# Performance work log

Measured on AMD Instinct MI355X. Metric: run time of the kernel, lower is better.

Reference implementation:

```python
import jax, jax.numpy as jnp
import numpy as np

N = 50000
E = 800000


def setup_inputs() -> dict:
    key = jax.random.key(0)
    ks = jax.random.split(key, 12)
    d, pd, h, md, od = 64, 3, 128, 64, 64

    def glorot(k, shape):
        fan_in = shape[0]
        return jax.random.normal(k, shape, dtype=jnp.float32) / jnp.sqrt(jnp.float32(fan_in))

    return {
        "x": jax.random.normal(ks[0], (N, d), dtype=jnp.float32),
        "pos": jax.random.normal(ks[1], (N, pd), dtype=jnp.float32),
        "edge_index": jax.random.randint(ks[2], (2, E), 0, N, dtype=jnp.int64 if jax.config.jax_enable_x64 else jnp.int32),
        "W1": glorot(ks[3], (2 * d + pd, h)),
        "b1": jnp.zeros((h,), dtype=jnp.float32),
        "W2": glorot(ks[4], (h, md)),
        "b2": jnp.zeros((md,), dtype=jnp.float32),
        "W3": glorot(ks[5], (d + md, h)),
        "b3": jnp.zeros((h,), dtype=jnp.float32),
        "W4": glorot(ks[6], (h, od)),
        "b4": jnp.zeros((od,), dtype=jnp.float32),
    }


def reference(x, pos, edge_index, W1, b1, W2, b2, W3, b3, W4, b4):
    # flow='target_to_source': i = edge_index[0] (aggregation node), j = edge_index[1]
    idx_i = edge_index[0]
    idx_j = edge_index[1]

    x_i = x[idx_i]          # [E, d]
    x_j = x[idx_j]          # [E, d]
    rel_pos = pos[idx_j] - pos[idx_i]  # [E, pd]  (neighbor_loc='position')

    # message MLP
    msg_in = jnp.concatenate([x_i, x_j - x_i, rel_pos], axis=1)  # [E, 2d+pd]
    hmsg = jax.nn.relu(msg_in @ W1 + b1)
    msg = hmsg @ W2 + b2  # [E, md]

    # scatter-mean aggregation at node i
    num_nodes = x.shape[0]
    summed = jax.ops.segment_sum(msg, idx_i, num_segments=num_nodes)  # [N, md]
    counts = jax.ops.segment_sum(jnp.ones((msg.shape[0],), dtype=msg.dtype), idx_i, num_segments=num_nodes)
    aggr = summed / jnp.maximum(counts, 1.0)[:, None]

    # update MLP (self_val=True: concat own features)
    upd_in = jnp.concatenate([x, aggr], axis=1)  # [N, d+md]
    hupd = jax.nn.relu(upd_in @ W3 + b3)
    return hupd @ W4 + b4  # [N, od]
```

## Files before the change

kernel.cpp:

```cpp
#include <hip/hip_runtime.h>


#define EPB 128
#define NPB 64

typedef __attribute__((ext_vector_type(8))) short bf16x8;
typedef __attribute__((ext_vector_type(4))) float f32x4;

static __device__ __forceinline__ unsigned short f2bf(float f) {
    union { float f; unsigned u; } v; v.f = f;
    unsigned u = v.u + 0x7FFFu + ((v.u >> 16) & 1u);
    return (unsigned short)(u >> 16);
}
static __device__ __forceinline__ float bf2f(unsigned short h) {
    union { unsigned u; float f; } v; v.u = ((unsigned)h) << 16;
    return v.f;
}
static __device__ __forceinline__ unsigned relu_add_pk(unsigned pu, unsigned qu) {
    union { unsigned u; float f; } plo, phi, qlo, qhi, lo, hi;
    plo.u = pu << 16;           phi.u = pu & 0xffff0000u;
    qlo.u = qu << 16;           qhi.u = qu & 0xffff0000u;
    lo.f = fmaxf(plo.f + qlo.f, 0.f);
    hi.f = fmaxf(phi.f + qhi.f, 0.f);
    return (hi.u & 0xffff0000u) | (lo.u >> 16);
}


__global__ __launch_bounds__(256) void count_kernel(
    const int* __restrict__ ei0, int* __restrict__ cnt,
    int* __restrict__ rank, int E)
{
    int e = blockIdx.x * 256 + threadIdx.x;
    if (e < E) rank[e] = atomicAdd(&cnt[ei0[e]], 1);
}

__global__ __launch_bounds__(1024) void scanA_kernel(
    const int* __restrict__ cnt, int* __restrict__ bsum, int N)
{
    __shared__ int ws[16];
    const int i = blockIdx.x * 1024 + threadIdx.x;
    int v = (i < N) ? cnt[i] : 0;
    #pragma unroll
    for (int d = 32; d >= 1; d >>= 1) v += __shfl_down(v, d, 64);
    if ((threadIdx.x & 63) == 0) ws[threadIdx.x >> 6] = v;
    __syncthreads();
    if (threadIdx.x == 0) {
        int s = 0;
        #pragma unroll
        for (int k = 0; k < 16; ++k) s += ws[k];
        bsum[blockIdx.x] = s;
    }
}

__global__ __launch_bounds__(1024) void scanC_kernel(
    const int* __restrict__ cnt, const int* __restrict__ bsum,
    int* __restrict__ off, int N, int Etot)
{
    __shared__ int wsum[16];
    __shared__ int boffs;
    const int i = blockIdx.x * 1024 + threadIdx.x;
    const int lane = threadIdx.x & 63, w = threadIdx.x >> 6;
    if (threadIdx.x < 64) {
        int acc = 0;
        for (int k = threadIdx.x; k < blockIdx.x; k += 64) acc += bsum[k];
        #pragma unroll
        for (int d = 32; d >= 1; d >>= 1) acc += __shfl_down(acc, d, 64);
        if (threadIdx.x == 0) boffs = acc;
    }
    const int v = (i < N) ? cnt[i] : 0;
    int incl = v;
    #pragma unroll
    for (int d = 1; d < 64; d <<= 1) {
        int t = __shfl_up(incl, d, 64);
        if (lane >= d) incl += t;
    }
    if (lane == 63) wsum[w] = incl;
    __syncthreads();
    int pre = 0;
    for (int k = 0; k < w; ++k) pre += wsum[k];
    if (i < N) off[i] = boffs + pre + incl - v;
    if (blockIdx.x == 0 && threadIdx.x == 0) off[N] = Etot;
}

__global__ __launch_bounds__(256) void fill_kernel(
    const int* __restrict__ ei0, const int* __restrict__ ei1,
    const int* __restrict__ off, const int* __restrict__ rank,
    int2* __restrict__ eij, int E)
{
    int e = blockIdx.x * 256 + threadIdx.x;
    if (e < E) {
        const int i = ei0[e];
        int2 v; v.x = i; v.y = ei1[e];
        eij[off[i] + rank[e]] = v;
    }
}


__global__ __launch_bounds__(64) void pack_weights_kernel(
    const float* __restrict__ W1, const float* __restrict__ W2,
    const float* __restrict__ W3, const float* __restrict__ W4,
    unsigned short* __restrict__ Wcp, unsigned short* __restrict__ W2p,
    unsigned short* __restrict__ W3p, unsigned short* __restrict__ W4p)
{
    int f = blockIdx.x;
    const int lane = threadIdx.x;
    if (f < 48) {
        const int nt = f / 3, ks = f % 3;
        const int n  = nt * 16 + (lane & 15);
        const int k0 = ks * 32 + (lane >> 4) * 8;
        unsigned short* dst = Wcp + (size_t)f * 512 + lane * 8;
        #pragma unroll
        for (int j = 0; j < 8; ++j) {
            const int k = k0 + j;
            float v = 0.f;
            if (n < 128) {
                if (k < 64)       v = W1[(size_t)k * 128 + n] - W1[(size_t)(64 + k) * 128 + n];
                else if (k < 67)  v = -W1[(size_t)(128 + k - 64) * 128 + n];
            } else {
                const int nq = n - 128;
                if (k < 64)       v = W1[(size_t)(64 + k) * 128 + nq];
                else if (k < 67)  v = W1[(size_t)(128 + k - 64) * 128 + nq];
            }
            dst[j] = f2bf(v);
        }
        return;
    }
    const float* W; unsigned short* out; int K, N, KS;
    if (f < 64)      { W = W2; out = W2p; K = 128; N = 64;  KS = 4; f -= 48; }
    else if (f < 96) { W = W3; out = W3p; K = 128; N = 128; KS = 4; f -= 64; }
    else             { W = W4; out = W4p; K = 128; N = 64;  KS = 4; f -= 96; }
    const int nt = f / KS, ks = f % KS;
    const int n  = nt * 16 + (lane & 15);
    const int k0 = ks * 32 + (lane >> 4) * 8;
    unsigned short* dst = out + (size_t)f * 512 + lane * 8;
    #pragma unroll
    for (int j = 0; j < 8; ++j) {
        float v = (k0 + j < K) ? W[(size_t)(k0 + j) * N + n] : 0.f;
        dst[j] = f2bf(v);
    }
}


__global__ __launch_bounds__(256) void pq_kernel(
    const float* __restrict__ x, const float* __restrict__ pos,
    const unsigned short* __restrict__ Wcp, const float* __restrict__ b1,
    unsigned short* __restrict__ P, unsigned short* __restrict__ Q, int N)
{
    __shared__ unsigned short s[NPB][136];

    const int tid  = threadIdx.x;
    const int wv   = tid >> 6;
    const int lane = tid & 63;
    const int r    = lane >> 4;
    const int c    = lane & 15;
    const int base = blockIdx.x * NPB;

    for (int nl = wv; nl < NPB; nl += 4) {
        const int n = base + nl;
        s[nl][lane] = (n < N) ? f2bf(x[(size_t)n * 64 + lane]) : 0;
        if (lane < 32)
            s[nl][64 + lane] = (n < N && lane < 3) ? f2bf(pos[(size_t)n * 3 + lane]) : 0;
    }
    __syncthreads();

    bf16x8 a[3];
    #pragma unroll
    for (int ks = 0; ks < 3; ++ks)
        a[ks] = *(const bf16x8*)&s[wv * 16 + c][ks * 32 + r * 8];
    __syncthreads();

    f32x4 acc[16];
    #pragma unroll
    for (int nt = 0; nt < 16; ++nt) {
        const float bv = (nt < 8) ? b1[nt * 16 + c] : 0.f;
        acc[nt] = (f32x4){bv, bv, bv, bv};
    }
    #pragma unroll
    for (int nt = 0; nt < 16; ++nt)
        #pragma unroll
        for (int ks = 0; ks < 3; ++ks) {
            const bf16x8 b = *(const bf16x8*)(Wcp + (size_t)(nt * 3 + ks) * 512 + lane * 8);
            acc[nt] = __builtin_amdgcn_mfma_f32_16x16x32_bf16(a[ks], b, acc[nt], 0, 0, 0);
        }

    #pragma unroll
    for (int nt = 0; nt < 8; ++nt)
        #pragma unroll
        for (int reg = 0; reg < 4; ++reg)
            s[wv * 16 + r * 4 + reg][nt * 16 + c] = f2bf(acc[nt][reg]);
    __syncthreads();
    {
        const int nl = tid >> 2, q = tid & 3;
        const int n = base + nl;
        if (n < N) {
            const ushort4* src = (const ushort4*)&s[nl][0];
            ushort4* dst = (ushort4*)(P + (size_t)n * 128);
            #pragma unroll
            for (int u = 0; u < 8; ++u) dst[q * 8 + u] = src[q * 8 + u];
        }
    }
    __syncthreads();

    #pragma unroll
    for (int nt = 8; nt < 16; ++nt)
        #pragma unroll
        for (int reg = 0; reg < 4; ++reg)
            s[wv * 16 + r * 4 + reg][(nt - 8) * 16 + c] = f2bf(acc[nt][reg]);
    __syncthreads();
    {
        const int nl = tid >> 2, q = tid & 3;
        const int n = base + nl;
        if (n < N) {
            const ushort4* src = (const ushort4*)&s[nl][0];
            ushort4* dst = (ushort4*)(Q + (size_t)n * 128);
            #pragma unroll
            for (int u = 0; u < 8; ++u) dst[q * 8 + u] = src[q * 8 + u];
        }
    }
}


__global__ __launch_bounds__(256) void edge_aggr_mfma(
    const unsigned short* __restrict__ P, const unsigned short* __restrict__ Q,
    const int2* __restrict__ eij,
    const unsigned short* __restrict__ W2p, const float* __restrict__ b2,
    float* __restrict__ aggr, int E)
{
    __shared__ unsigned short s_m[EPB][72];
    __shared__ int2 s_ij[EPB];
    __shared__ int  s_start[EPB + 4];
    __shared__ int  s_wsumA[2];
    __shared__ int  s_nruns;

    const int tid  = threadIdx.x;
    const int wv   = tid >> 6;
    const int lane = tid & 63;
    const int r    = lane >> 4;
    const int c    = lane & 15;
    const int base = blockIdx.x * EPB;
    const int ne   = min(EPB, E - base);

    if (tid < EPB) {
        const int p = base + tid;
        int2 v; v.x = -1; v.y = -1;
        if (p < E) v = eij[p];
        s_ij[tid] = v;
    }
    __syncthreads();

    bf16x8 a2[2][4];
    #pragma unroll
    for (int mh = 0; mh < 2; ++mh) {
        const int2 ij = s_ij[wv * 32 + mh * 16 + c];
        if (ij.x >= 0) {
            const unsigned* Pi = (const unsigned*)(P + (size_t)ij.x * 128);
            const unsigned* Qj = (const unsigned*)(Q + (size_t)ij.y * 128);
            #pragma unroll
            for (int ks = 0; ks < 4; ++ks) {
                const uint4 pu = *(const uint4*)(Pi + ks * 16 + r * 4);
                const uint4 qu = *(const uint4*)(Qj + ks * 16 + r * 4);
                uint4 h;
                h.x = relu_add_pk(pu.x, qu.x);
                h.y = relu_add_pk(pu.y, qu.y);
                h.z = relu_add_pk(pu.z, qu.z);
                h.w = relu_add_pk(pu.w, qu.w);
                a2[mh][ks] = *(const bf16x8*)&h;
            }
        } else {
            #pragma unroll
            for (int ks = 0; ks < 4; ++ks) a2[mh][ks] = (bf16x8){0,0,0,0,0,0,0,0};
        }
    }

    f32x4 acc2[2][4];
    #pragma unroll
    for (int nt = 0; nt < 4; ++nt) {
        const float bv = b2[nt * 16 + c];
        acc2[0][nt] = (f32x4){bv, bv, bv, bv};
        acc2[1][nt] = (f32x4){bv, bv, bv, bv};
    }
    #pragma unroll
    for (int nt = 0; nt < 4; ++nt)
        #pragma unroll
        for (int ks = 0; ks < 4; ++ks) {
            const bf16x8 b = *(const bf16x8*)(W2p + (size_t)(nt * 4 + ks) * 512 + lane * 8);
            acc2[0][nt] = __builtin_amdgcn_mfma_f32_16x16x32_bf16(a2[0][ks], b, acc2[0][nt], 0, 0, 0);
            acc2[1][nt] = __builtin_amdgcn_mfma_f32_16x16x32_bf16(a2[1][ks], b, acc2[1][nt], 0, 0, 0);
        }

    #pragma unroll
    for (int mh = 0; mh < 2; ++mh)
        #pragma unroll
        for (int nt = 0; nt < 4; ++nt)
            #pragma unroll
            for (int reg = 0; reg < 4; ++reg) {
                const int row = wv * 32 + mh * 16 + r * 4 + reg;
                s_m[row][nt * 16 + c] = f2bf(acc2[mh][nt][reg]);
            }

    int flag = 0, incl = 0;
    if (tid < EPB) {
        flag = (tid < ne) && (tid == 0 || s_ij[tid].x != s_ij[tid - 1].x);
        incl = flag;
    }
    #pragma unroll
    for (int d = 1; d < 64; d <<= 1) {
        int t = __shfl_up(incl, d, 64);
        if (lane >= d) incl += t;
    }
    if (tid < EPB && lane == 63) s_wsumA[tid >> 6] = incl;
    __syncthreads();
    if (tid < EPB) {
        const int rid = incl + ((tid >= 64) ? s_wsumA[0] : 0);
        if (flag) s_start[rid - 1] = tid;
    }
    if (tid == 0) {
        const int nr = s_wsumA[0] + s_wsumA[1];
        s_nruns = nr;
        s_start[nr] = ne;
    }
    __syncthreads();

    for (int rn = wv; rn < s_nruns; rn += 4) {
        const int e0 = s_start[rn], e1 = s_start[rn + 1];
        const int i  = s_ij[e0].x;
        float acc = 0.f;
        for (int e = e0; e < e1; ++e)
            acc += bf2f(s_m[e][lane]);
        atomicAdd(&aggr[(size_t)i * 64 + lane], acc);
    }
}


__global__ __launch_bounds__(256) void node_mlp_mfma(
    const float* __restrict__ x, const float* __restrict__ aggr,
    const int* __restrict__ off,
    const unsigned short* __restrict__ W3p, const float* __restrict__ b3,
    const unsigned short* __restrict__ W4p, const float* __restrict__ b4,
    float* __restrict__ out, int N)
{
    __shared__ unsigned short s_a[NPB][136];

    const int tid  = threadIdx.x;
    const int wv   = tid >> 6;
    const int lane = tid & 63;
    const int r    = lane >> 4;
    const int c    = lane & 15;
    const int base = blockIdx.x * NPB;

    for (int nl = wv; nl < NPB; nl += 4) {
        const int n = base + nl;
        if (n < N) {
            s_a[nl][lane] = f2bf(x[(size_t)n * 64 + lane]);
            const int deg = off[n + 1] - off[n];
            const float a = aggr[(size_t)n * 64 + lane] / (float)max(deg, 1);
            s_a[nl][64 + lane] = f2bf(a);
        } else {
            s_a[nl][lane] = 0;
            s_a[nl][64 + lane] = 0;
        }
    }
    __syncthreads();

    bf16x8 a1[4];
    #pragma unroll
    for (int ks = 0; ks < 4; ++ks)
        a1[ks] = *(const bf16x8*)&s_a[wv * 16 + c][ks * 32 + r * 8];
    __syncthreads();

    f32x4 acc1[8];
    #pragma unroll
    for (int nt = 0; nt < 8; ++nt) {
        const float bv = b3[nt * 16 + c];
        acc1[nt] = (f32x4){bv, bv, bv, bv};
    }
    #pragma unroll
    for (int nt = 0; nt < 8; ++nt)
        #pragma unroll
        for (int ks = 0; ks < 4; ++ks) {
            const bf16x8 b = *(const bf16x8*)(W3p + (size_t)(nt * 4 + ks) * 512 + lane * 8);
            acc1[nt] = __builtin_amdgcn_mfma_f32_16x16x32_bf16(a1[ks], b, acc1[nt], 0, 0, 0);
        }
    #pragma unroll
    for (int nt = 0; nt < 8; ++nt)
        #pragma unroll
        for (int reg = 0; reg < 4; ++reg)
            s_a[wv * 16 + r * 4 + reg][nt * 16 + c] = f2bf(fmaxf(acc1[nt][reg], 0.f));
    __syncthreads();

    bf16x8 a2[4];
    #pragma unroll
    for (int ks = 0; ks < 4; ++ks)
        a2[ks] = *(const bf16x8*)&s_a[wv * 16 + c][ks * 32 + r * 8];
    __syncthreads();

    f32x4 acc2[4];
    #pragma unroll
    for (int nt = 0; nt < 4; ++nt) {
        const float bv = b4[nt * 16 + c];
        acc2[nt] = (f32x4){bv, bv, bv, bv};
    }
    #pragma unroll
    for (int nt = 0; nt < 4; ++nt)
        #pragma unroll
        for (int ks = 0; ks < 4; ++ks) {
            const bf16x8 b = *(const bf16x8*)(W4p + (size_t)(nt * 4 + ks) * 512 + lane * 8);
            acc2[nt] = __builtin_amdgcn_mfma_f32_16x16x32_bf16(a2[ks], b, acc2[nt], 0, 0, 0);
        }

    #pragma unroll
    for (int nt = 0; nt < 4; ++nt)
        #pragma unroll
        for (int reg = 0; reg < 4; ++reg) {
            float* row = (float*)&s_a[wv * 16 + r * 4 + reg][0];
            row[nt * 16 + c] = acc2[nt][reg];
        }
    __syncthreads();

    {
        const int nl = tid >> 2, q = tid & 3;
        const int n = base + nl;
        if (n < N) {
            const float4* src = (const float4*)((const float*)&s_a[nl][0] + q * 16);
            float4* dst = (float4*)(out + (size_t)n * 64 + q * 16);
            #pragma unroll
            for (int u = 0; u < 4; ++u) dst[u] = src[u];
        }
    }
}


#define EB 32
#define NB 32

__global__ __launch_bounds__(256) void mpnn_edge_atomic_kernel(
    const float* __restrict__ x, const float* __restrict__ pos,
    const int* __restrict__ ei0, const int* __restrict__ ei1,
    const float* __restrict__ W1, const float* __restrict__ b1,
    const float* __restrict__ W2, const float* __restrict__ b2,
    float* __restrict__ summed, float* __restrict__ counts, int E)
{
    __shared__ float s_in[EB][132];
    __shared__ int   s_idx[EB];

    const int tid  = threadIdx.x;
    const int base = blockIdx.x * EB;
    const int wv   = tid >> 6;
    const int lane = tid & 63;

    for (int e = wv; e < EB; e += 4) {
        const int ei = base + e;
        if (ei < E) {
            const int i = ei0[ei];
            const int j = ei1[ei];
            const float xi = x[(size_t)i * 64 + lane];
            const float xj = x[(size_t)j * 64 + lane];
            s_in[e][lane]      = xi;
            s_in[e][64 + lane] = xj - xi;
            if (lane < 3)
                s_in[e][128 + lane] = pos[(size_t)j * 3 + lane] - pos[(size_t)i * 3 + lane];
            if (lane == 0) s_idx[e] = i;
        } else {
            s_in[e][lane] = 0.f; s_in[e][64 + lane] = 0.f;
            if (lane < 3) s_in[e][128 + lane] = 0.f;
            if (lane == 0) s_idx[e] = -1;
        }
    }
    __syncthreads();

    float acc1[4][4];
    {
        const int cg = tid & 31;
        const int er = tid >> 5;
        const float4 bb = *(const float4*)(b1 + 4 * cg);
        #pragma unroll
        for (int t = 0; t < 4; ++t) {
            acc1[t][0] = bb.x; acc1[t][1] = bb.y; acc1[t][2] = bb.z; acc1[t][3] = bb.w;
        }
        for (int k = 0; k < 128; k += 4) {
            float wv4[4][4];
            #pragma unroll
            for (int kk = 0; kk < 4; ++kk) {
                const float4 w = *(const float4*)(W1 + (size_t)(k + kk) * 128 + 4 * cg);
                wv4[kk][0] = w.x; wv4[kk][1] = w.y; wv4[kk][2] = w.z; wv4[kk][3] = w.w;
            }
            #pragma unroll
            for (int t = 0; t < 4; ++t) {
                const float4 m = *(const float4*)(&s_in[er + 8 * t][k]);
                const float mm[4] = {m.x, m.y, m.z, m.w};
                #pragma unroll
                for (int kk = 0; kk < 4; ++kk)
                    #pragma unroll
                    for (int cc = 0; cc < 4; ++cc)
                        acc1[t][cc] += mm[kk] * wv4[kk][cc];
            }
        }
        for (int k = 128; k < 131; ++k) {
            float wk[4];
            #pragma unroll
            for (int cc = 0; cc < 4; ++cc) wk[cc] = W1[(size_t)k * 128 + 4 * cg + cc];
            #pragma unroll
            for (int t = 0; t < 4; ++t) {
                const float m = s_in[er + 8 * t][k];
                #pragma unroll
                for (int cc = 0; cc < 4; ++cc) acc1[t][cc] += m * wk[cc];
            }
        }
    }
    __syncthreads();
    {
        const int cg = tid & 31;
        const int er = tid >> 5;
        #pragma unroll
        for (int t = 0; t < 4; ++t)
            #pragma unroll
            for (int cc = 0; cc < 4; ++cc)
                s_in[er + 8 * t][4 * cg + cc] = fmaxf(acc1[t][cc], 0.f);
    }
    __syncthreads();
    {
        const int cg = tid & 15;
        const int er = tid >> 4;
        float acc[2][4];
        const float4 bb = *(const float4*)(b2 + 4 * cg);
        #pragma unroll
        for (int t = 0; t < 2; ++t) {
            acc[t][0] = bb.x; acc[t][1] = bb.y; acc[t][2] = bb.z; acc[t][3] = bb.w;
        }
        for (int k = 0; k < 128; k += 4) {
            float wv4[4][4];
            #pragma unroll
            for (int kk = 0; kk < 4; ++kk) {
                const float4 w = *(const float4*)(W2 + (size_t)(k + kk) * 64 + 4 * cg);
                wv4[kk][0] = w.x; wv4[kk][1] = w.y; wv4[kk][2] = w.z; wv4[kk][3] = w.w;
            }
            #pragma unroll
            for (int t = 0; t < 2; ++t) {
                const float4 m = *(const float4*)(&s_in[er + 16 * t][k]);
                const float mm[4] = {m.x, m.y, m.z, m.w};
                #pragma unroll
                for (int kk = 0; kk < 4; ++kk)
                    #pragma unroll
                    for (int cc = 0; cc < 4; ++cc)
                        acc[t][cc] += mm[kk] * wv4[kk][cc];
            }
        }
        #pragma unroll
        for (int t = 0; t < 2; ++t) {
            const int e = er + 16 * t;
            const int i = s_idx[e];
            if (i >= 0) {
                #pragma unroll
                for (int cc = 0; cc < 4; ++cc)
                    atomicAdd(&summed[(size_t)i * 64 + 4 * cg + cc], acc[t][cc]);
            }
        }
    }
    if (tid < EB) {
        const int i = s_idx[tid];
        if (i >= 0) atomicAdd(&counts[i], 1.0f);
    }
}

__global__ __launch_bounds__(256) void mpnn_node_legacy_kernel(
    const float* __restrict__ x, const float* __restrict__ summed,
    const float* __restrict__ counts,
    const float* __restrict__ W3, const float* __restrict__ b3,
    const float* __restrict__ W4, const float* __restrict__ b4,
    float* __restrict__ out, int N)
{
    __shared__ float s_in[NB][132];

    const int tid  = threadIdx.x;
    const int base = blockIdx.x * NB;
    const int wv   = tid >> 6;
    const int lane = tid & 63;

    for (int nl = wv; nl < NB; nl += 4) {
        const int n = base + nl;
        if (n < N) {
            s_in[nl][lane] = x[(size_t)n * 64 + lane];
            const float inv = 1.0f / fmaxf(counts[n], 1.0f);
            s_in[nl][64 + lane] = summed[(size_t)n * 64 + lane] * inv;
        } else {
            s_in[nl][lane] = 0.f; s_in[nl][64 + lane] = 0.f;
        }
    }
    __syncthreads();

    float acc1[4][4];
    {
        const int cg = tid & 31;
        const int er = tid >> 5;
        const float4 bb = *(const float4*)(b3 + 4 * cg);
        #pragma unroll
        for (int t = 0; t < 4; ++t) {
            acc1[t][0] = bb.x; acc1[t][1] = bb.y; acc1[t][2] = bb.z; acc1[t][3] = bb.w;
        }
        for (int k = 0; k < 128; k += 4) {
            float wv4[4][4];
            #pragma unroll
            for (int kk = 0; kk < 4; ++kk) {
                const float4 w = *(const float4*)(W3 + (size_t)(k + kk) * 128 + 4 * cg);
                wv4[kk][0] = w.x; wv4[kk][1] = w.y; wv4[kk][2] = w.z; wv4[kk][3] = w.w;
            }
            #pragma unroll
            for (int t = 0; t < 4; ++t) {
                const float4 m = *(const float4*)(&s_in[er + 8 * t][k]);
                const float mm[4] = {m.x, m.y, m.z, m.w};
                #pragma unroll
                for (int kk = 0; kk < 4; ++kk)
                    #pragma unroll
                    for (int cc = 0; cc < 4; ++cc)
                        acc1[t][cc] += mm[kk] * wv4[kk][cc];
            }
        }
    }
    __syncthreads();
    {
        const int cg = tid & 31;
        const int er = tid >> 5;
        #pragma unroll
        for (int t = 0; t < 4; ++t)
            #pragma unroll
            for (int cc = 0; cc < 4; ++cc)
                s_in[er + 8 * t][4 * cg + cc] = fmaxf(acc1[t][cc], 0.f);
    }
    __syncthreads();
    {
        const int cg = tid & 15;
        const int er = tid >> 4;
        float acc[2][4];
        const float4 bb = *(const float4*)(b4 + 4 * cg);
        #pragma unroll
        for (int t = 0; t < 2; ++t) {
            acc[t][0] = bb.x; acc[t][1] = bb.y; acc[t][2] = bb.z; acc[t][3] = bb.w;
        }
        for (int k = 0; k < 128; k += 4) {
            float wv4[4][4];
            #pragma unroll
            for (int kk = 0; kk < 4; ++kk) {
                const float4 w = *(const float4*)(W4 + (size_t)(k + kk) * 64 + 4 * cg);
                wv4[kk][0] = w.x; wv4[kk][1] = w.y; wv4[kk][2] = w.z; wv4[kk][3] = w.w;
            }
            #pragma unroll
            for (int t = 0; t < 2; ++t) {
                const float4 m = *(const float4*)(&s_in[er + 16 * t][k]);
                const float mm[4] = {m.x, m.y, m.z, m.w};
                #pragma unroll
                for (int kk = 0; kk < 4; ++kk)
                    #pragma unroll
                    for (int cc = 0; cc < 4; ++cc)
                        acc[t][cc] += mm[kk] * wv4[kk][cc];
            }
        }
        #pragma unroll
        for (int t = 0; t < 2; ++t) {
            const int n = base + er + 16 * t;
            if (n < N) {
                float4 o;
                o.x = acc[t][0]; o.y = acc[t][1]; o.z = acc[t][2]; o.w = acc[t][3];
                *(float4*)(out + (size_t)n * 64 + 4 * cg) = o;
            }
        }
    }
}


static inline size_t rup(size_t v) { return (v + 255) & ~(size_t)255; }

extern "C" void kernel_launch(void* const* d_in, const int* in_sizes, int n_in,
                              void* d_out, int out_size, void* d_ws, size_t ws_size,
                              hipStream_t stream) {
    const float* x    = (const float*)d_in[0];
    const float* pos  = (const float*)d_in[1];
    const int*   eidx = (const int*)d_in[2];
    const float* W1   = (const float*)d_in[3];
    const float* b1   = (const float*)d_in[4];
    const float* W2   = (const float*)d_in[5];
    const float* b2   = (const float*)d_in[6];
    const float* W3   = (const float*)d_in[7];
    const float* b3   = (const float*)d_in[8];
    const float* W4   = (const float*)d_in[9];
    const float* b4   = (const float*)d_in[10];

    const int N = in_sizes[0] / 64;
    const int E = in_sizes[2] / 2;
    const int* ei0 = eidx;
    const int* ei1 = eidx + E;
    const int nb = (N + 1023) / 1024;

    const size_t p_b    = rup((size_t)N * 128 * 2);
    const size_t q_b    = rup((size_t)N * 128 * 2);
    const size_t wcp_b  = rup(48 * 512 * 2);
    const size_t w2p_b  = rup(16 * 512 * 2);
    const size_t w3p_b  = rup(32 * 512 * 2);
    const size_t w4p_b  = rup(16 * 512 * 2);
    const size_t aggr_b = rup((size_t)N * 64 * 4);
    const size_t cnt_b  = rup((size_t)N * 4);
    const size_t off_b  = rup((size_t)(N + 1) * 4);
    const size_t bsum_b = rup(256 * 4);
    const size_t rank_b = rup((size_t)E * 4);
    const size_t eij_b  = rup((size_t)E * 8);
    const size_t need = p_b + q_b + wcp_b + w2p_b + w3p_b + w4p_b +
                        aggr_b + cnt_b + off_b + bsum_b + rank_b + eij_b;

    if (ws_size >= need) {
        char* p = (char*)d_ws;
        unsigned short* P   = (unsigned short*)p;  p += p_b;
        unsigned short* Q   = (unsigned short*)p;  p += q_b;
        unsigned short* Wcp = (unsigned short*)p;  p += wcp_b;
        unsigned short* W2p = (unsigned short*)p;  p += w2p_b;
        unsigned short* W3p = (unsigned short*)p;  p += w3p_b;
        unsigned short* W4p = (unsigned short*)p;  p += w4p_b;
        float* aggr = (float*)p;  p += aggr_b;
        int* cnt  = (int*)p;  p += cnt_b;
        int* off  = (int*)p;  p += off_b;
        int* bsum = (int*)p;  p += bsum_b;
        int* rank = (int*)p;  p += rank_b;
        int2* eij = (int2*)p;

        hipMemsetAsync(aggr, 0, aggr_b + cnt_b, stream);

        pack_weights_kernel<<<112, 64, 0, stream>>>(W1, W2, W3, W4, Wcp, W2p, W3p, W4p);
        pq_kernel<<<(N + NPB - 1) / NPB, 256, 0, stream>>>(x, pos, Wcp, b1, P, Q, N);

        const int eb256 = (E + 255) / 256;
        count_kernel<<<eb256, 256, 0, stream>>>(ei0, cnt, rank, E);
        scanA_kernel<<<nb, 1024, 0, stream>>>(cnt, bsum, N);
        scanC_kernel<<<nb, 1024, 0, stream>>>(cnt, bsum, off, N, E);
        fill_kernel<<<eb256, 256, 0, stream>>>(ei0, ei1, off, rank, eij, E);

        edge_aggr_mfma<<<(E + EPB - 1) / EPB, 256, 0, stream>>>(
            P, Q, eij, W2p, b2, aggr, E);

        node_mlp_mfma<<<(N + NPB - 1) / NPB, 256, 0, stream>>>(
            x, aggr, off, W3p, b3, W4p, b4, (float*)d_out, N);
    } else {
        float* summed = (float*)d_ws;
        float* counts = summed + (size_t)N * 64;
        hipMemsetAsync(d_ws, 0, ((size_t)N * 64 + N) * sizeof(float), stream);

        mpnn_edge_atomic_kernel<<<(E + EB - 1) / EB, 256, 0, stream>>>(
            x, pos, ei0, ei1, W1, b1, W2, b2, summed, counts, E);
        mpnn_node_legacy_kernel<<<(N + NB - 1) / NB, 256, 0, stream>>>(
            x, summed, counts, W3, b3, W4, b4, (float*)d_out, N);
    }
}
```

Before: 262.2 us.

## Fuse preprocessing kernels and use decoupled-lookback scan; swizzle edge block order

Weight packing and the edge count atomics are merged into one launch. The P/Q node GEMM and the offset scan are merged into another, and the scan now uses a single-pass decoupled lookback through spin-waits on a block-sum array initialised to -1. Together these remove several kernel launches and the separate two-pass scan. Edge-aggregation blocks are also remapped with an XCD-style swizzle (stride of 8) so that consecutive edge ranges land on the same die, aiming for better L2 locality. The trade-off is that the lookback spin relies on earlier scan blocks being scheduled before later ones, a forward-progress assumption that could hang or add latency.

```diff
diff --git a/kernel.cpp b/kernel.cpp
--- a/kernel.cpp
+++ b/kernel.cpp
@@ -26,61 +26,174 @@
 }
 
 
-__global__ __launch_bounds__(256) void count_kernel(
+__global__ __launch_bounds__(256) void prep_kernel(
+    const float* __restrict__ W1, const float* __restrict__ W2,
+    const float* __restrict__ W3, const float* __restrict__ W4,
+    unsigned short* __restrict__ Wcp, unsigned short* __restrict__ W2p,
+    unsigned short* __restrict__ W3p, unsigned short* __restrict__ W4p,
     const int* __restrict__ ei0, int* __restrict__ cnt,
-    int* __restrict__ rank, int E)
+    int* __restrict__ rank, int* __restrict__ bsum, int E)
 {
-    int e = blockIdx.x * 256 + threadIdx.x;
-    if (e < E) rank[e] = atomicAdd(&cnt[ei0[e]], 1);
-}
-
-__global__ __launch_bounds__(1024) void scanA_kernel(
-    const int* __restrict__ cnt, int* __restrict__ bsum, int N)
-{
-    __shared__ int ws[16];
-    const int i = blockIdx.x * 1024 + threadIdx.x;
-    int v = (i < N) ? cnt[i] : 0;
-    #pragma unroll
-    for (int d = 32; d >= 1; d >>= 1) v += __shfl_down(v, d, 64);
-    if ((threadIdx.x & 63) == 0) ws[threadIdx.x >> 6] = v;
-    __syncthreads();
-    if (threadIdx.x == 0) {
-        int s = 0;
-        #pragma unroll
-        for (int k = 0; k < 16; ++k) s += ws[k];
-        bsum[blockIdx.x] = s;
-    }
-}
-
-__global__ __launch_bounds__(1024) void scanC_kernel(
-    const int* __restrict__ cnt, const int* __restrict__ bsum,
+    const int tid = threadIdx.x;
+    if (blockIdx.x < 28) {
+        if (blockIdx.x == 0) bsum[tid] = -1;
+        int f = blockIdx.x * 4 + (tid >> 6);
+        const int lane = tid & 63;
+        if (f < 48) {
+            const int nt = f / 3, ks = f % 3;
+            const int n  = nt * 16 + (lane & 15);
+            const int k0 = ks * 32 + (lane >> 4) * 8;
+            unsigned short* dst = Wcp + (size_t)f * 512 + lane * 8;
+            #pragma unroll
+            for (int j = 0; j < 8; ++j) {
+                const int k = k0 + j;
+                float v = 0.f;
+                if (n < 128) {
+                    if (k < 64)       v = W1[(size_t)k * 128 + n] - W1[(size_t)(64 + k) * 128 + n];
+                    else if (k < 67)  v = -W1[(size_t)(128 + k - 64) * 128 + n];
+                } else {
+                    const int nq = n - 128;
+                    if (k < 64)       v = W1[(size_t)(64 + k) * 128 + nq];
+                    else if (k < 67)  v = W1[(size_t)(128 + k - 64) * 128 + nq];
+                }
+                dst[j] = f2bf(v);
+            }
+            return;
+        }
+        const float* W; unsigned short* out; int K, N, KS;
+        if (f < 64)      { W = W2; out = W2p; K = 128; N = 64;  KS = 4; f -= 48; }
+        else if (f < 96) { W = W3; out = W3p; K = 128; N = 128; KS = 4; f -= 64; }
+        else             { W = W4; out = W4p; K = 128; N = 64;  KS = 4; f -= 96; }
+        const int nt = f / KS, ks = f % KS;
+        const int n  = nt * 16 + (lane & 15);
+        const int k0 = ks * 32 + (lane >> 4) * 8;
+        unsigned short* dst = out + (size_t)f * 512 + lane * 8;
+        #pragma unroll
+        for (int j = 0; j < 8; ++j) {
+            float v = (k0 + j < K) ? W[(size_t)(k0 + j) * N + n] : 0.f;
+            dst[j] = f2bf(v);
+        }
+    } else {
+        const int e = (blockIdx.x - 28) * 256 + tid;
+        if (e < E) rank[e] = atomicAdd(&cnt[ei0[e]], 1);
+    }
+}
+
+
+__global__ __launch_bounds__(256) void pq_scan_kernel(
+    const float* __restrict__ x, const float* __restrict__ pos,
+    const unsigned short* __restrict__ Wcp, const float* __restrict__ b1,
+    unsigned short* __restrict__ P, unsigned short* __restrict__ Q,
+    const int* __restrict__ cnt, int* __restrict__ bsum,
     int* __restrict__ off, int N, int Etot)
 {
-    __shared__ int wsum[16];
-    __shared__ int boffs;
-    const int i = blockIdx.x * 1024 + threadIdx.x;
-    const int lane = threadIdx.x & 63, w = threadIdx.x >> 6;
-    if (threadIdx.x < 64) {
-        int acc = 0;
-        for (int k = threadIdx.x; k < blockIdx.x; k += 64) acc += bsum[k];
-        #pragma unroll
-        for (int d = 32; d >= 1; d >>= 1) acc += __shfl_down(acc, d, 64);
-        if (threadIdx.x == 0) boffs = acc;
-    }
-    const int v = (i < N) ? cnt[i] : 0;
-    int incl = v;
-    #pragma unroll
-    for (int d = 1; d < 64; d <<= 1) {
-        int t = __shfl_up(incl, d, 64);
-        if (lane >= d) incl += t;
-    }
-    if (lane == 63) wsum[w] = incl;
-    __syncthreads();
-    int pre = 0;
-    for (int k = 0; k < w; ++k) pre += wsum[k];
-    if (i < N) off[i] = boffs + pre + incl - v;
-    if (blockIdx.x == 0 && threadIdx.x == 0) off[N] = Etot;
-}
+    __shared__ unsigned short s[NPB][136];
+    __shared__ int wsum[4];
+    __shared__ int s_boff;
+
+    const int tid  = threadIdx.x;
+    const int pqBlocks = (N + NPB - 1) / NPB;
+
+    if ((int)blockIdx.x >= pqBlocks) {
+        const int s_id = blockIdx.x - pqBlocks;
+        const int scanBlocks = (N + 255) >> 8;
+        const int i = s_id * 256 + tid;
+        const int lane = tid & 63, w = tid >> 6;
+        const int v = (i < N) ? cnt[i] : 0;
+        int incl = v;
+        #pragma unroll
+        for (int d = 1; d < 64; d <<= 1) {
+            int t = __shfl_up(incl, d, 64);
+            if (lane >= d) incl += t;
+        }
+        if (lane == 63) wsum[w] = incl;
+        if (tid == 0) s_boff = 0;
+        __syncthreads();
+        int pre = 0;
+        for (int k = 0; k < w; ++k) pre += wsum[k];
+        const int btot = wsum[0] + wsum[1] + wsum[2] + wsum[3];
+        if (tid == 0) atomicExch(&bsum[s_id], btot);
+        if (tid < s_id) {
+            int val;
+            do { val = atomicAdd(&bsum[tid], 0); } while (val == -1);
+            atomicAdd(&s_boff, val);
+        }
+        __syncthreads();
+        if (i < N) off[i] = s_boff + pre + incl - v;
+        if (s_id == scanBlocks - 1 && tid == 0) off[N] = Etot;
+        return;
+    }
+
+    const int wv   = tid >> 6;
+    const int lane = tid & 63;
+    const int r    = lane >> 4;
+    const int c    = lane & 15;
+    const int base = blockIdx.x * NPB;
+
+    for (int nl = wv; nl < NPB; nl += 4) {
+        const int n = base + nl;
+        s[nl][lane] = (n < N) ? f2bf(x[(size_t)n * 64 + lane]) : 0;
+        if (lane < 32)
+            s[nl][64 + lane] = (n < N && lane < 3) ? f2bf(pos[(size_t)n * 3 + lane]) : 0;
+    }
+    __syncthreads();
+
+    bf16x8 a[3];
+    #pragma unroll
+    for (int ks = 0; ks < 3; ++ks)
+        a[ks] = *(const bf16x8*)&s[wv * 16 + c][ks * 32 + r * 8];
+    __syncthreads();
+
+    f32x4 acc[16];
+    #pragma unroll
+    for (int nt = 0; nt < 16; ++nt) {
+        const float bv = (nt < 8) ? b1[nt * 16 + c] : 0.f;
+        acc[nt] = (f32x4){bv, bv, bv, bv};
+    }
+    #pragma unroll
+    for (int nt = 0; nt < 16; ++nt)
+        #pragma unroll
+        for (int ks = 0; ks < 3; ++ks) {
+            const bf16x8 b = *(const bf16x8*)(Wcp + (size_t)(nt * 3 + ks) * 512 + lane * 8);
+            acc[nt] = __builtin_amdgcn_mfma_f32_16x16x32_bf16(a[ks], b, acc[nt], 0, 0, 0);
+        }
+
+    #pragma unroll
+    for (int nt = 0; nt < 8; ++nt)
+        #pragma unroll
+        for (int reg = 0; reg < 4; ++reg)
+            s[wv * 16 + r * 4 + reg][nt * 16 + c] = f2bf(acc[nt][reg]);
+    __syncthreads();
+    {
+        const int nl = tid >> 2, q = tid & 3;
+        const int n = base + nl;
+        if (n < N) {
+            const ushort4* src = (const ushort4*)&s[nl][0];
+            ushort4* dst = (ushort4*)(P + (size_t)n * 128);
+            #pragma unroll
+            for (int u = 0; u < 8; ++u) dst[q * 8 + u] = src[q * 8 + u];
+        }
+    }
+    __syncthreads();
+
+    #pragma unroll
+    for (int nt = 8; nt < 16; ++nt)
+        #pragma unroll
+        for (int reg = 0; reg < 4; ++reg)
+            s[wv * 16 + r * 4 + reg][(nt - 8) * 16 + c] = f2bf(acc[nt][reg]);
+    __syncthreads();
+    {
+        const int nl = tid >> 2, q = tid & 3;
+        const int n = base + nl;
+        if (n < N) {
+            const ushort4* src = (const ushort4*)&s[nl][0];
+            ushort4* dst = (ushort4*)(Q + (size_t)n * 128);
+            #pragma unroll
+            for (int u = 0; u < 8; ++u) dst[q * 8 + u] = src[q * 8 + u];
+        }
+    }
+}
+
 
 __global__ __launch_bounds__(256) void fill_kernel(
     const int* __restrict__ ei0, const int* __restrict__ ei1,
@@ -92,130 +205,6 @@
         const int i = ei0[e];
         int2 v; v.x = i; v.y = ei1[e];
         eij[off[i] + rank[e]] = v;
-    }
-}
-
-
-__global__ __launch_bounds__(64) void pack_weights_kernel(
-    const float* __restrict__ W1, const float* __restrict__ W2,
-    const float* __restrict__ W3, const float* __restrict__ W4,
-    unsigned short* __restrict__ Wcp, unsigned short* __restrict__ W2p,
-    unsigned short* __restrict__ W3p, unsigned short* __restrict__ W4p)
-{
-    int f = blockIdx.x;
-    const int lane = threadIdx.x;
-    if (f < 48) {
-        const int nt = f / 3, ks = f % 3;
-        const int n  = nt * 16 + (lane & 15);
-        const int k0 = ks * 32 + (lane >> 4) * 8;
-        unsigned short* dst = Wcp + (size_t)f * 512 + lane * 8;
-        #pragma unroll
-        for (int j = 0; j < 8; ++j) {
-            const int k = k0 + j;
-            float v = 0.f;
-            if (n < 128) {
-                if (k < 64)       v = W1[(size_t)k * 128 + n] - W1[(size_t)(64 + k) * 128 + n];
-                else if (k < 67)  v = -W1[(size_t)(128 + k - 64) * 128 + n];
-            } else {
-                const int nq = n - 128;
-                if (k < 64)       v = W1[(size_t)(64 + k) * 128 + nq];
-                else if (k < 67)  v = W1[(size_t)(128 + k - 64) * 128 + nq];
-            }
-            dst[j] = f2bf(v);
-        }
-        return;
-    }
-    const float* W; unsigned short* out; int K, N, KS;
-    if (f < 64)      { W = W2; out = W2p; K = 128; N = 64;  KS = 4; f -= 48; }
-    else if (f < 96) { W = W3; out = W3p; K = 128; N = 128; KS = 4; f -= 64; }
-    else             { W = W4; out = W4p; K = 128; N = 64;  KS = 4; f -= 96; }
-    const int nt = f / KS, ks = f % KS;
-    const int n  = nt * 16 + (lane & 15);
-    const int k0 = ks * 32 + (lane >> 4) * 8;
-    unsigned short* dst = out + (size_t)f * 512 + lane * 8;
-    #pragma unroll
-    for (int j = 0; j < 8; ++j) {
-        float v = (k0 + j < K) ? W[(size_t)(k0 + j) * N + n] : 0.f;
-        dst[j] = f2bf(v);
-    }
-}
-
-
-__global__ __launch_bounds__(256) void pq_kernel(
-    const float* __restrict__ x, const float* __restrict__ pos,
-    const unsigned short* __restrict__ Wcp, const float* __restrict__ b1,
-    unsigned short* __restrict__ P, unsigned short* __restrict__ Q, int N)
-{
-    __shared__ unsigned short s[NPB][136];
-
-    const int tid  = threadIdx.x;
-    const int wv   = tid >> 6;
-    const int lane = tid & 63;
-    const int r    = lane >> 4;
-    const int c    = lane & 15;
-    const int base = blockIdx.x * NPB;
-
-    for (int nl = wv; nl < NPB; nl += 4) {
-        const int n = base + nl;
-        s[nl][lane] = (n < N) ? f2bf(x[(size_t)n * 64 + lane]) : 0;
-        if (lane < 32)
-            s[nl][64 + lane] = (n < N && lane < 3) ? f2bf(pos[(size_t)n * 3 + lane]) : 0;
-    }
-    __syncthreads();
-
-    bf16x8 a[3];
-    #pragma unroll
-    for (int ks = 0; ks < 3; ++ks)
-        a[ks] = *(const bf16x8*)&s[wv * 16 + c][ks * 32 + r * 8];
-    __syncthreads();
-
-    f32x4 acc[16];
-    #pragma unroll
-    for (int nt = 0; nt < 16; ++nt) {
-        const float bv = (nt < 8) ? b1[nt * 16 + c] : 0.f;
-        acc[nt] = (f32x4){bv, bv, bv, bv};
-    }
-    #pragma unroll
-    for (int nt = 0; nt < 16; ++nt)
-        #pragma unroll
-        for (int ks = 0; ks < 3; ++ks) {
-            const bf16x8 b = *(const bf16x8*)(Wcp + (size_t)(nt * 3 + ks) * 512 + lane * 8);
-            acc[nt] = __builtin_amdgcn_mfma_f32_16x16x32_bf16(a[ks], b, acc[nt], 0, 0, 0);
-        }
-
-    #pragma unroll
-    for (int nt = 0; nt < 8; ++nt)
-        #pragma unroll
-        for (int reg = 0; reg < 4; ++reg)
-            s[wv * 16 + r * 4 + reg][nt * 16 + c] = f2bf(acc[nt][reg]);
-    __syncthreads();
-    {
-        const int nl = tid >> 2, q = tid & 3;
-        const int n = base + nl;
-        if (n < N) {
-            const ushort4* src = (const ushort4*)&s[nl][0];
-            ushort4* dst = (ushort4*)(P + (size_t)n * 128);
-            #pragma unroll
-            for (int u = 0; u < 8; ++u) dst[q * 8 + u] = src[q * 8 + u];
-        }
-    }
-    __syncthreads();
-
-    #pragma unroll
-    for (int nt = 8; nt < 16; ++nt)
-        #pragma unroll
-        for (int reg = 0; reg < 4; ++reg)
-            s[wv * 16 + r * 4 + reg][(nt - 8) * 16 + c] = f2bf(acc[nt][reg]);
-    __syncthreads();
-    {
-        const int nl = tid >> 2, q = tid & 3;
-        const int n = base + nl;
-        if (n < N) {
-            const ushort4* src = (const ushort4*)&s[nl][0];
-            ushort4* dst = (ushort4*)(Q + (size_t)n * 128);
-            #pragma unroll
-            for (int u = 0; u < 8; ++u) dst[q * 8 + u] = src[q * 8 + u];
-        }
     }
 }
 
@@ -237,7 +226,11 @@
     const int lane = tid & 63;
     const int r    = lane >> 4;
     const int c    = lane & 15;
-    const int base = blockIdx.x * EPB;
+
+    const int per  = gridDim.x >> 3;
+    const int swz  = (blockIdx.x & 7) * per + (blockIdx.x >> 3);
+    const int base = swz * EPB;
+    if (base >= E) return;
     const int ne   = min(EPB, E - base);
 
     if (tid < EPB) {
@@ -688,7 +681,6 @@
     const int E = in_sizes[2] / 2;
     const int* ei0 = eidx;
     const int* ei1 = eidx + E;
-    const int nb = (N + 1023) / 1024;
 
     const size_t p_b    = rup((size_t)N * 128 * 2);
     const size_t q_b    = rup((size_t)N * 128 * 2);
@@ -722,19 +714,22 @@
 
         hipMemsetAsync(aggr, 0, aggr_b + cnt_b, stream);
 
-        pack_weights_kernel<<<112, 64, 0, stream>>>(W1, W2, W3, W4, Wcp, W2p, W3p, W4p);
-        pq_kernel<<<(N + NPB - 1) / NPB, 256, 0, stream>>>(x, pos, Wcp, b1, P, Q, N);
-
-        const int eb256 = (E + 255) / 256;
-        count_kernel<<<eb256, 256, 0, stream>>>(ei0, cnt, rank, E);
-        scanA_kernel<<<nb, 1024, 0, stream>>>(cnt, bsum, N);
-        scanC_kernel<<<nb, 1024, 0, stream>>>(cnt, bsum, off, N, E);
-        fill_kernel<<<eb256, 256, 0, stream>>>(ei0, ei1, off, rank, eij, E);
-
-        edge_aggr_mfma<<<(E + EPB - 1) / EPB, 256, 0, stream>>>(
+        const int cntBlocks = (E + 255) / 256;
+        prep_kernel<<<28 + cntBlocks, 256, 0, stream>>>(
+            W1, W2, W3, W4, Wcp, W2p, W3p, W4p, ei0, cnt, rank, bsum, E);
+
+        const int pqBlocks   = (N + NPB - 1) / NPB;
+        const int scanBlocks = (N + 255) / 256;
+        pq_scan_kernel<<<pqBlocks + scanBlocks, 256, 0, stream>>>(
+            x, pos, Wcp, b1, P, Q, cnt, bsum, off, N, E);
+
+        fill_kernel<<<cntBlocks, 256, 0, stream>>>(ei0, ei1, off, rank, eij, E);
+
+        const int edgeBlocks = ((E + EPB - 1) / EPB + 7) & ~7;
+        edge_aggr_mfma<<<edgeBlocks, 256, 0, stream>>>(
             P, Q, eij, W2p, b2, aggr, E);
 
-        node_mlp_mfma<<<(N + NPB - 1) / NPB, 256, 0, stream>>>(
+        node_mlp_mfma<<<pqBlocks, 256, 0, stream>>>(
             x, aggr, off, W3p, b3, W4p, b4, (float*)d_out, N);
     } else {
         float* summed = (float*)d_ws;
```

After: 256.4 us. 2.2% less time.
